# Performance work log

Measured on AMD Instinct MI355X. Metric: run time of the kernel, lower is better.

The kernel has to match this reference:

```python
import jax, jax.numpy as jnp
import numpy as np

VOCAB = 100000
HIDDEN = 512
NUM_CLUSTERS = 256
B, S = 8, 2048


def setup_inputs() -> dict:
    key = jax.random.key(0)
    k1, k2, k3, k4, k5 = jax.random.split(key, 5)
    return {
        "location_ids": jax.random.randint(k1, (B, S), 0, VOCAB),
        "fine_embed_w": jax.random.normal(k2, (VOCAB, HIDDEN // 2), dtype=jnp.float32),
        "coarse_embed_w": jax.random.normal(k3, (NUM_CLUSTERS, HIDDEN // 2), dtype=jnp.float32),
        "loc_to_cluster_w": jax.random.normal(k4, (NUM_CLUSTERS, VOCAB), dtype=jnp.float32),
        "loc_to_cluster_b": jax.random.normal(k5, (NUM_CLUSTERS,), dtype=jnp.float32),
    }


def reference(location_ids, fine_embed_w, coarse_embed_w, loc_to_cluster_w, loc_to_cluster_b):
    # fine embedding gather: [B,S,H/2]
    fine_emb = fine_embed_w[location_ids]
    # one_hot(ids) @ W^T + b  ==  gather columns of W at ids, plus bias
    # cluster_logits: [B,S,C]
    cluster_logits = loc_to_cluster_w.T[location_ids] + loc_to_cluster_b
    cluster_dist = jax.nn.softmax(cluster_logits, axis=-1)
    # soft mixture of coarse cluster embeddings: [B,S,H/2]
    coarse_emb = jnp.einsum("bsc,ch->bsh", cluster_dist, coarse_embed_w)
    return jnp.concatenate([fine_emb, coarse_emb], axis=-1)
```

## Files before the change

### kernel.cpp

```cpp
#include <hip/hip_runtime.h>
#include <hip/hip_bf16.h>

#define VOCAB 100000
#define HALF  256
#define NC    256
#define NTOK  16384
#define SEGSZ 3200
#define NSEG  32
#define NHB   16

using frag  = __attribute__((ext_vector_type(8))) short;
using f32x4 = __attribute__((ext_vector_type(4))) float;

static __device__ inline unsigned bfpk(float lo, float hi) {
    union { __hip_bfloat162 h2; unsigned u; } cv;
    cv.h2.x = __float2bfloat16(lo);
    cv.h2.y = __float2bfloat16(hi);
    return cv.u;
}

__global__ __launch_bounds__(1024)
void prep1(const int* __restrict__ ids, const float* __restrict__ coarse_w,
           int* __restrict__ partial, ushort* __restrict__ cT)
{
    __shared__ float tile[64][65];
    __shared__ int lh[NSEG];
    const int tid = threadIdx.x;
    const int b   = blockIdx.x;

    if (b < NHB) {
        if (tid < NSEG) lh[tid] = 0;
        __syncthreads();
        atomicAdd(&lh[ids[b * 1024 + tid] / SEGSZ], 1);
        __syncthreads();
        if (tid < NSEG) partial[b * NSEG + tid] = lh[tid];
    } else {
        const int bt = b - NHB;
        const int ci = (bt >> 2) * 64, hi = (bt & 3) * 64;
#pragma unroll
        for (int p = 0; p < 4; ++p) {
            const int idx = tid + p * 1024;
            const int cl = idx >> 6, hl = idx & 63;
            tile[cl][hl] = coarse_w[(size_t)(ci + cl) * HALF + hi + hl];
        }
        __syncthreads();
#pragma unroll
        for (int p = 0; p < 4; ++p) {
            const int idx = tid + p * 1024;
            const int hl = idx >> 6, cl = idx & 63;
            __hip_bfloat16 v = __float2bfloat16(tile[cl][hl]);
            cT[(size_t)(hi + hl) * NC + ci + cl] = *reinterpret_cast<ushort*>(&v);
        }
    }
}

__global__ __launch_bounds__(1024)
void prep2(const int* __restrict__ ids, const int* __restrict__ partial,
           int* __restrict__ seg_off, int* __restrict__ stok, int* __restrict__ sidv)
{
    __shared__ int part_l[NHB][NSEG];
    __shared__ int segoff[NSEG + 1];
    __shared__ int basebs[NSEG];
    __shared__ int cnt[NSEG];
    const int tid = threadIdx.x;
    const int b   = blockIdx.x;

    if (tid < NHB * NSEG) part_l[tid >> 5][tid & 31] = partial[tid];
    __syncthreads();

    if (tid < NSEG) {
        int tot_before = 0;
        int tot_s = 0;
        int base  = 0;
        for (int bb = 0; bb < NHB; ++bb) {
            const int v = part_l[bb][tid];
            tot_s += v;
            if (bb < b) base += v;
        }
        for (int s = 0; s < NSEG; ++s) {
            if (s < tid) {
                for (int bb = 0; bb < NHB; ++bb) tot_before += part_l[bb][s];
            }
        }
        segoff[tid] = tot_before;
        basebs[tid] = base;
        cnt[tid]    = 0;
        if (tid == NSEG - 1) segoff[NSEG] = tot_before + tot_s;
    }
    __syncthreads();

    const int t  = b * 1024 + tid;
    const int id = ids[t];
    const int sg = id / SEGSZ;
    const int r  = atomicAdd(&cnt[sg], 1);
    const int pos = segoff[sg] + basebs[sg] + r;
    stok[pos] = t;
    sidv[pos] = id;

    if (b == 0 && tid <= NSEG) seg_off[tid] = segoff[tid];
}

__global__ __launch_bounds__(256)
void gather_rows(const float* __restrict__ cluster_w,
                 const float* __restrict__ cluster_b,
                 const int*   __restrict__ sidv,
                 const int*   __restrict__ seg_off,
                 __hip_bfloat16* __restrict__ logT)
{
    __shared__ float seg[SEGSZ];
    const int bid = blockIdx.x;
    const int r   = bid >> 5;
    const int s   = bid & 31;
    const int tid = threadIdx.x;
    const int sbase = s * SEGSZ;
    const int slen  = min(SEGSZ, VOCAB - sbase);

    const float4* src = reinterpret_cast<const float4*>(cluster_w + (size_t)r * VOCAB + sbase);
    float4* dst = reinterpret_cast<float4*>(seg);
    const int nf4 = slen >> 2;
    for (int i = tid; i < nf4; i += 256) dst[i] = src[i];

    const float bias = cluster_b[r];
    const int lo = seg_off[s];
    const int hi = seg_off[s + 1];
    __syncthreads();

    for (int i = lo + tid; i < hi; i += 256) {
        const int id = sidv[i];
        logT[(size_t)r * NTOK + i] = __float2bfloat16(seg[id - sbase] + bias);
    }
}

__global__ __launch_bounds__(512)
void mix_mfma(const ushort* __restrict__ logT,
              const float*  __restrict__ fine_w,
              const ushort* __restrict__ cT,
              const int*    __restrict__ stok,
              const int*    __restrict__ sidv,
              float*        __restrict__ out)
{
    __shared__ uint4 ldsA[32][33];
    __shared__ float redu[32][17];
    __shared__ int stok_l[32], sid_l[32];

    const int tid  = threadIdx.x;
    const int base = blockIdx.x * 32;

    if (tid < 32) { stok_l[tid] = stok[base + tid]; sid_l[tid] = sidv[base + tid]; }

    const int s = tid & 31;
    const int g = tid >> 5;
    float v[16];
#pragma unroll
    for (int i = 0; i < 16; ++i) {
        const unsigned u = logT[(size_t)(g * 16 + i) * NTOK + base + s];
        v[i] = __uint_as_float(u << 16);
    }
    float m = v[0];
#pragma unroll
    for (int i = 1; i < 16; ++i) m = fmaxf(m, v[i]);
    redu[s][g] = m;
    __syncthreads();
    float M = redu[s][0];
#pragma unroll
    for (int i = 1; i < 16; ++i) M = fmaxf(M, redu[s][i]);
    __syncthreads();
    float sum = 0.f;
#pragma unroll
    for (int i = 0; i < 16; ++i) { v[i] = __expf(v[i] - M); sum += v[i]; }
    redu[s][g] = sum;
    __syncthreads();
    float tot = 0.f;
#pragma unroll
    for (int i = 0; i < 16; ++i) tot += redu[s][i];
    const float inv = 1.f / tot;

    {
        uint4 u0, u1;
        u0.x = bfpk(v[0] * inv,  v[1] * inv);
        u0.y = bfpk(v[2] * inv,  v[3] * inv);
        u0.z = bfpk(v[4] * inv,  v[5] * inv);
        u0.w = bfpk(v[6] * inv,  v[7] * inv);
        u1.x = bfpk(v[8] * inv,  v[9] * inv);
        u1.y = bfpk(v[10] * inv, v[11] * inv);
        u1.z = bfpk(v[12] * inv, v[13] * inv);
        u1.w = bfpk(v[14] * inv, v[15] * inv);
        ldsA[s][2 * g]     = u0;
        ldsA[s][2 * g + 1] = u1;
    }

    {
        const int sl = tid >> 4, l16 = tid & 15;
        const float4* fs = reinterpret_cast<const float4*>(fine_w + (size_t)sid_l[sl] * HALF);
        float4* fd = reinterpret_cast<float4*>(out + (size_t)stok_l[sl] * 512);
#pragma unroll
        for (int p = 0; p < 4; ++p) fd[l16 + 16 * p] = fs[l16 + 16 * p];
    }
    __syncthreads();

    const int w    = tid >> 6;
    const int lane = tid & 63;
    const int arow = (w & 1) * 16 + (lane & 15);
    const int ngrp = (w >> 1) * 4;
    f32x4 acc[4];
#pragma unroll
    for (int q = 0; q < 4; ++q) acc[q] = (f32x4){0.f, 0.f, 0.f, 0.f};

    for (int ch = 0; ch < 8; ++ch) {
        const frag a = *reinterpret_cast<const frag*>(&ldsA[arow][ch * 4 + (lane >> 4)]);
#pragma unroll
        for (int q = 0; q < 4; ++q) {
            const int n = (ngrp + q) * 16 + (lane & 15);
            const frag b = *reinterpret_cast<const frag*>(
                cT + (size_t)n * NC + ch * 32 + (lane >> 4) * 8);
            acc[q] = __builtin_amdgcn_mfma_f32_16x16x32_bf16(a, b, acc[q], 0, 0, 0);
        }
    }

#pragma unroll
    for (int q = 0; q < 4; ++q) {
        const int col = (ngrp + q) * 16 + (lane & 15);
#pragma unroll
        for (int r = 0; r < 4; ++r) {
            const int srow = (w & 1) * 16 + (lane >> 4) * 4 + r;
            out[(size_t)stok_l[srow] * 512 + 256 + col] = acc[q][r];
        }
    }
}

extern "C" void kernel_launch(void* const* d_in, const int* in_sizes, int n_in,
                              void* d_out, int out_size, void* d_ws, size_t ws_size,
                              hipStream_t stream) {
    const int*   ids       = (const int*)  d_in[0];
    const float* fine_w    = (const float*)d_in[1];
    const float* coarse_w  = (const float*)d_in[2];
    const float* cluster_w = (const float*)d_in[3];
    const float* cluster_b = (const float*)d_in[4];
    float*       out       = (float*)d_out;

    int* partial = (int*)d_ws;
    int* seg_off = partial + NHB * NSEG;
    int* stok    = seg_off + 64;
    int* sidv    = stok + NTOK;
    __hip_bfloat16* logT = (__hip_bfloat16*)(sidv + NTOK);
    ushort* cT = (ushort*)(logT + (size_t)NC * NTOK);

    const size_t need = (size_t)(NHB * NSEG + 64 + 2 * NTOK) * sizeof(int)
                      + (size_t)NC * NTOK * 2 + (size_t)HALF * NC * 2;
    if (ws_size < need) return;

    hipLaunchKernelGGL(prep1, dim3(2 * NHB), dim3(1024), 0, stream,
                       ids, coarse_w, partial, cT);
    hipLaunchKernelGGL(prep2, dim3(NHB), dim3(1024), 0, stream,
                       ids, partial, seg_off, stok, sidv);
    hipLaunchKernelGGL(gather_rows, dim3(NC * NSEG), dim3(256), 0, stream,
                       cluster_w, cluster_b, sidv, seg_off, logT);
    hipLaunchKernelGGL(mix_mfma, dim3(NTOK / 32), dim3(512), 0, stream,
                       (const ushort*)logT, fine_w, cT, stok, sidv, out);
}
```

Before: 58.16 us.

## Process four vocab segments per gather block with register-prefetched next segment

Result: slower. 85.59 us (+47.2%).

```diff
diff --git a/kernel.cpp b/kernel.cpp
--- a/kernel.cpp
+++ b/kernel.cpp
@@ -69,19 +69,15 @@
     __syncthreads();
 
     if (tid < NSEG) {
-        int tot_before = 0;
-        int tot_s = 0;
-        int base  = 0;
+        int tot_before = 0, tot_s = 0, base = 0;
         for (int bb = 0; bb < NHB; ++bb) {
             const int v = part_l[bb][tid];
             tot_s += v;
             if (bb < b) base += v;
         }
-        for (int s = 0; s < NSEG; ++s) {
-            if (s < tid) {
+        for (int s = 0; s < NSEG; ++s)
+            if (s < tid)
                 for (int bb = 0; bb < NHB; ++bb) tot_before += part_l[bb][s];
-            }
-        }
         segoff[tid] = tot_before;
         basebs[tid] = base;
         cnt[tid]    = 0;
@@ -108,26 +104,47 @@
                  __hip_bfloat16* __restrict__ logT)
 {
     __shared__ float seg[SEGSZ];
-    const int bid = blockIdx.x;
-    const int r   = bid >> 5;
-    const int s   = bid & 31;
     const int tid = threadIdx.x;
-    const int sbase = s * SEGSZ;
-    const int slen  = min(SEGSZ, VOCAB - sbase);
-
-    const float4* src = reinterpret_cast<const float4*>(cluster_w + (size_t)r * VOCAB + sbase);
-    float4* dst = reinterpret_cast<float4*>(seg);
-    const int nf4 = slen >> 2;
-    for (int i = tid; i < nf4; i += 256) dst[i] = src[i];
-
+    const int r   = blockIdx.x >> 3;
+    const int e   = blockIdx.x & 7;
     const float bias = cluster_b[r];
-    const int lo = seg_off[s];
-    const int hi = seg_off[s + 1];
-    __syncthreads();
-
-    for (int i = lo + tid; i < hi; i += 256) {
-        const int id = sidv[i];
-        logT[(size_t)r * NTOK + i] = __float2bfloat16(seg[id - sbase] + bias);
+    const float* rowp = cluster_w + (size_t)r * VOCAB;
+
+    int s     = e * 4;
+    int sbase = s * SEGSZ;
+    int nf4   = min(SEGSZ, VOCAB - sbase) >> 2;
+
+    float4 pf[4];
+#pragma unroll
+    for (int p = 0; p < 4; ++p) {
+        const int i = tid + p * 256;
+        if (i < nf4) pf[p] = *reinterpret_cast<const float4*>(rowp + sbase + 4 * i);
+    }
+
+    for (int k = 0; k < 4; ++k, ++s) {
+#pragma unroll
+        for (int p = 0; p < 4; ++p) {
+            const int i = tid + p * 256;
+            if (i < nf4) *reinterpret_cast<float4*>(&seg[4 * i]) = pf[p];
+        }
+        const int sb_cur = sbase;
+        const int lo = seg_off[s];
+        const int hi = seg_off[s + 1];
+
+        if (k < 3) {
+            sbase += SEGSZ;
+            nf4 = min(SEGSZ, VOCAB - sbase) >> 2;
+#pragma unroll
+            for (int p = 0; p < 4; ++p) {
+                const int i = tid + p * 256;
+                if (i < nf4) pf[p] = *reinterpret_cast<const float4*>(rowp + sbase + 4 * i);
+            }
+        }
+        __syncthreads();
+
+        for (int i = lo + tid; i < hi; i += 256)
+            logT[(size_t)r * NTOK + i] = __float2bfloat16(seg[sidv[i] - sb_cur] + bias);
+        __syncthreads();
     }
 }
 
@@ -253,7 +270,7 @@
                        ids, coarse_w, partial, cT);
     hipLaunchKernelGGL(prep2, dim3(NHB), dim3(1024), 0, stream,
                        ids, partial, seg_off, stok, sidv);
-    hipLaunchKernelGGL(gather_rows, dim3(NC * NSEG), dim3(256), 0, stream,
+    hipLaunchKernelGGL(gather_rows, dim3(NC * 8), dim3(256), 0, stream,
                        cluster_w, cluster_b, sidv, seg_off, logT);
     hipLaunchKernelGGL(mix_mfma, dim3(NTOK / 32), dim3(512), 0, stream,
                        (const ushort*)logT, fine_w, cT, stok, sidv, out);
```
